# Optimization experiments

Measured on AMD Instinct MI355X. Metric: run time of the kernel, lower is better.

Reference implementation:

```python
import jax, jax.numpy as jnp
import numpy as np

# dims: L=seq_len, N=batch, C=embed_dim, H=heads, D=head_dim, W=window_size
L, N, C, H, D, W = 1024, 4, 2048, 16, 128, 512
ROPE_BASE = 10000.0
SCALE = 1.0 / np.sqrt(D).astype(np.float32)


def _rope(x, cos, sin):
    # interleaved-pair rotary embedding; x: (..., D), cos/sin broadcast to (..., D//2)
    x1, x2 = x[..., 0::2], x[..., 1::2]
    return jnp.stack([x1 * cos - x2 * sin, x1 * sin + x2 * cos], axis=-1).reshape(x.shape)


def setup_inputs() -> dict:
    key = jax.random.key(0)
    ks = jax.random.split(key, 4)
    s = 0.02
    return {
        "x": jax.random.normal(ks[0], (L, N, C), jnp.float32),
        "wq": jax.random.normal(ks[1], (C, C), jnp.float32) * s,
        "bq": jnp.zeros((C,), jnp.float32),
        "wkv": jax.random.normal(ks[2], (2 * C, C), jnp.float32) * s,
        "bkv": jnp.zeros((2 * C,), jnp.float32),
        "wo": jax.random.normal(ks[3], (C, C), jnp.float32) * s,
        "bo": jnp.zeros((C,), jnp.float32),
        "alibi_slopes": jnp.asarray(2.0 ** (-8.0 * np.arange(1, H + 1) / H), jnp.float32),
    }


def reference(x, wq, bq, wkv, bkv, wo, bo, alibi_slopes):
    # x: (L, N, C) -> batch-major (N, L, C)
    xb = jnp.transpose(x, (1, 0, 2))
    q = (xb @ wq.T + bq).reshape(N, L, H, D)
    # memory=None path: zero input cache, cache_mask all False
    cache = jnp.zeros((N, W, C), x.dtype)
    kv_cache = cache @ wkv.T + bkv          # detached in original; masked out anyway
    kv_cur = xb @ wkv.T + bkv
    kv = jnp.concatenate([kv_cache, kv_cur], axis=1).reshape(N, L + W, 2, H, D)
    # RoPE over absolute kv positions [0, L+W); queries live at positions [W, W+L)
    t = jnp.arange(L + W, dtype=jnp.float32)
    inv_freq = 1.0 / (ROPE_BASE ** (jnp.arange(0, D, 2, dtype=jnp.float32) / D))
    freqs = jnp.outer(t, inv_freq)          # (L+W, D//2)
    cos, sin = jnp.cos(freqs), jnp.sin(freqs)
    q = _rope(q, cos[W:W + L][None, :, None, :], sin[W:W + L][None, :, None, :])
    k = _rope(kv[:, :, 0], cos[None, :, None, :], sin[None, :, None, :])
    v = kv[:, :, 1]
    scores = jnp.einsum('bihd,bjhd->bhij', q, k) * SCALE  # (N,H,L,L+W)
    i = jnp.arange(L)[:, None]
    j = jnp.arange(L + W)[None, :]
    # causal sliding window: query at kv-position i+W attends j in [i, i+W];
    # kv_mask is False for the (empty) cache region j < W
    mask = (j >= i) & (j <= i + W) & (j >= W)
    bias = alibi_slopes[:, None, None] * (j - i - W).astype(jnp.float32)  # <= 0 in window
    scores = jnp.where(mask[None, None], scores + bias[None], -jnp.inf)
    p = jax.nn.softmax(scores, axis=-1)
    attn = jnp.einsum('bhij,bjhd->bihd', p, v).reshape(N, L, C)
    out = attn @ wo.T + bo
    return jnp.transpose(out, (1, 0, 2))    # (L, N, C)
```

## Files before the change

### kernel.cpp

```cpp
#include <hip/hip_runtime.h>
#include <hip/hip_bf16.h>

typedef __attribute__((ext_vector_type(4))) float f32x4;
typedef __attribute__((ext_vector_type(8))) short s16x8;
typedef __attribute__((ext_vector_type(4))) short s16x4;
typedef __attribute__((ext_vector_type(4))) int i32x4;

__device__ __forceinline__ short f2bf(float f) {
    union { __hip_bfloat16 h; short s; } u;
    u.h = __float2bfloat16(f);
    return u.s;
}

#define GLD16(g, l) __builtin_amdgcn_global_load_lds((const __attribute__((address_space(1))) void*)(g), (__attribute__((address_space(3))) void*)(l), 16, 0, 0)
#define MFMA16(a, b, c) __builtin_amdgcn_mfma_f32_16x16x32_bf16((a), (b), (c), 0, 0, 0)

__global__ void conv_lin(const float* __restrict__ in, short* __restrict__ out, int n4) {
    int i = blockIdx.x * blockDim.x + threadIdx.x;
    int stride = gridDim.x * blockDim.x;
    for (; i < n4; i += stride) {
        float4 v = reinterpret_cast<const float4*>(in)[i];
        s16x4 o;
        o[0] = f2bf(v.x); o[1] = f2bf(v.y); o[2] = f2bf(v.z); o[3] = f2bf(v.w);
        reinterpret_cast<s16x4*>(out)[i] = o;
    }
}

__global__ void conv_x(const float* __restrict__ x, short* __restrict__ Xb) {
    const int total = 1024 * 4 * 2048 / 4;
    int i = blockIdx.x * blockDim.x + threadIdx.x;
    int stride = gridDim.x * blockDim.x;
    for (; i < total; i += stride) {
        float4 v = reinterpret_cast<const float4*>(x)[i];
        int c4 = i & 511;
        int n  = (i >> 9) & 3;
        int l  = i >> 11;
        s16x4 o;
        o[0] = f2bf(v.x); o[1] = f2bf(v.y); o[2] = f2bf(v.z); o[3] = f2bf(v.w);
        reinterpret_cast<s16x4*>(Xb)[(n * 1024 + l) * 512 + c4] = o;
    }
}

__global__ void rope_tab(float* __restrict__ ctab, float* __restrict__ stab) {
    int l = blockIdx.x, t = threadIdx.x;
    float pos = (float)(512 + l);
    float inv = __expf(-9.210340371976184f * ((float)t * (1.0f / 64.0f)));
    float a = pos * inv;
    float s, c;
    sincosf(a, &s, &c);
    ctab[l * 64 + t] = c;
    stab[l * 64 + t] = s;
}

__device__ __forceinline__ void gemm128(const short* __restrict__ A, const short* __restrict__ B,
                                        short* As, short* Bs, f32x4 acc[4][4], int m0, int j0) {
    const int K = 2048;
    const int tid = threadIdx.x;
    const int lane = tid & 63;
    const int w = tid >> 6;
    const int wr = w >> 1, wc = w & 1;
    const int r8 = lane >> 3;
    const int cc = ((lane & 7) ^ r8) << 3;
    const size_t rowA0 = (size_t)(m0 + w * 32 + r8);
    const size_t rowB0 = (size_t)(j0 + w * 32 + r8);
    for (int kt = 0; kt < K; kt += 64) {
        #pragma unroll
        for (int q = 0; q < 4; ++q) {
            GLD16(A + (rowA0 + q * 8) * K + kt + cc, As + (w * 32 + q * 8) * 64);
            GLD16(B + (rowB0 + q * 8) * K + kt + cc, Bs + (w * 32 + q * 8) * 64);
        }
        __syncthreads();
        #pragma unroll
        for (int kk = 0; kk < 2; ++kk) {
            s16x8 af[4], bfv[4];
            #pragma unroll
            for (int mi = 0; mi < 4; ++mi) {
                int row = wr * 64 + mi * 16 + (lane & 15);
                int byte = row * 128 + ((kk * 64 + (lane >> 4) * 16) ^ ((row & 7) << 4));
                af[mi] = *reinterpret_cast<const s16x8*>(reinterpret_cast<const char*>(As) + byte);
            }
            #pragma unroll
            for (int nj = 0; nj < 4; ++nj) {
                int row = wc * 64 + nj * 16 + (lane & 15);
                int byte = row * 128 + ((kk * 64 + (lane >> 4) * 16) ^ ((row & 7) << 4));
                bfv[nj] = *reinterpret_cast<const s16x8*>(reinterpret_cast<const char*>(Bs) + byte);
            }
            #pragma unroll
            for (int mi = 0; mi < 4; ++mi)
                #pragma unroll
                for (int nj = 0; nj < 4; ++nj)
                    acc[mi][nj] = MFMA16(af[mi], bfv[nj], acc[mi][nj]);
        }
        __syncthreads();
    }
}

__global__ __launch_bounds__(256, 2)
void gemm_qkv(const short* __restrict__ Xb, const short* __restrict__ Wqkv,
              const float* __restrict__ bq, const float* __restrict__ bkv,
              const float* __restrict__ ctab, const float* __restrict__ stab,
              short* __restrict__ Qr, short* __restrict__ Kr, short* __restrict__ Vr) {
    __shared__ short As[8192], Bs[8192];
    const int m0 = blockIdx.y * 128, j0 = blockIdx.x * 128;
    f32x4 acc[4][4];
    #pragma unroll
    for (int a = 0; a < 4; ++a)
        #pragma unroll
        for (int b = 0; b < 4; ++b)
            #pragma unroll
            for (int r = 0; r < 4; ++r) acc[a][b][r] = 0.f;
    gemm128(Xb, Wqkv, As, Bs, acc, m0, j0);

    const int tid = threadIdx.x, lane = tid & 63, w = tid >> 6;
    const int wr = w >> 1, wc = w & 1;
    const int region = j0 >> 11;
    #pragma unroll
    for (int mi = 0; mi < 4; ++mi) {
        #pragma unroll
        for (int nj = 0; nj < 4; ++nj) {
            int col = j0 + wc * 64 + nj * 16 + (lane & 15);
            int h = (col >> 7) & 15;
            int d = col & 127;
            #pragma unroll
            for (int r = 0; r < 4; ++r) {
                int row = m0 + wr * 64 + mi * 16 + (lane >> 4) * 4 + r;
                int n = row >> 10, l = row & 1023;
                float v = acc[mi][nj][r];
                size_t oidx = (((size_t)(n * 16 + h)) * 1024 + l) * 128 + d;
                if (region == 0) {
                    v += bq[col];
                    float other = __shfl_xor(v, 1, 64);
                    float cs = ctab[l * 64 + (d >> 1)];
                    float sn = stab[l * 64 + (d >> 1)];
                    float o = (d & 1) ? (other * sn + v * cs) : (v * cs - other * sn);
                    Qr[oidx] = f2bf(o * 0.08838834764831843f);
                } else if (region == 1) {
                    v += bkv[col - 2048];
                    float other = __shfl_xor(v, 1, 64);
                    float cs = ctab[l * 64 + (d >> 1)];
                    float sn = stab[l * 64 + (d >> 1)];
                    float o = (d & 1) ? (other * sn + v * cs) : (v * cs - other * sn);
                    Kr[oidx] = f2bf(o);
                } else {
                    v += bkv[col - 2048];
                    Vr[oidx] = f2bf(v);
                }
            }
        }
    }
}

__global__ __launch_bounds__(256, 1)
void attn_fwd(const short* __restrict__ Qr, const short* __restrict__ Kr,
              const short* __restrict__ Vr, const float* __restrict__ slopes,
              short* __restrict__ Attn) {
    __shared__ short Ks[64 * 128];
    __shared__ short Vts[128 * 64];
    __shared__ short Ps[4][2048];

    const int i0 = blockIdx.x * 128;
    const int nh = blockIdx.y;
    const int n = nh >> 4, h = nh & 15;
    const short* Qh = Qr + (size_t)nh * (1024 * 128);
    const short* Kh = Kr + (size_t)nh * (1024 * 128);
    const short* Vh = Vr + (size_t)nh * (1024 * 128);
    const float slope = slopes[h];
    const int tid = threadIdx.x, lane = tid & 63, w = tid >> 6;

    s16x8 qf[2][4];
    #pragma unroll
    for (int mi = 0; mi < 2; ++mi)
        #pragma unroll
        for (int kk = 0; kk < 4; ++kk) {
            int row = i0 + w * 32 + mi * 16 + (lane & 15);
            qf[mi][kk] = *reinterpret_cast<const s16x8*>(Qh + (size_t)row * 128 + kk * 32 + (lane >> 4) * 8);
        }

    f32x4 oacc[2][8];
    #pragma unroll
    for (int mi = 0; mi < 2; ++mi)
        #pragma unroll
        for (int dj = 0; dj < 8; ++dj)
            #pragma unroll
            for (int r = 0; r < 4; ++r) oacc[mi][dj][r] = 0.f;
    float mrun[2][4], lrun[2][4];
    #pragma unroll
    for (int mi = 0; mi < 2; ++mi)
        #pragma unroll
        for (int r = 0; r < 4; ++r) { mrun[mi][r] = -1e30f; lrun[mi][r] = 0.f; }

    const int jlo = (i0 >= 512) ? (i0 - 512) : 0;
    const int jhi = i0 + 127;
    for (int j0 = jlo; j0 <= jhi; j0 += 64) {
        #pragma unroll
        for (int q = 0; q < 4; ++q) {
            int rbase = w * 16 + q * 4;
            int rloc = rbase + (lane >> 4);
            int lc = ((lane & 15) ^ (rloc & 7)) << 3;
            GLD16(Kh + (size_t)(j0 + rloc) * 128 + lc, Ks + rbase * 128);
        }
        #pragma unroll
        for (int p = 0; p < 4; ++p) {
            int d0 = (w + p * 4) * 8;
            int jj = j0 + lane;
            i32x4 vv = *reinterpret_cast<const i32x4*>(Vh + (size_t)jj * 128 + d0);
            const short* vs = reinterpret_cast<const short*>(&vv);
            #pragma unroll
            for (int e = 0; e < 8; ++e) {
                int d = d0 + e;
                int byte = d * 128 + ((lane * 2) ^ ((d & 7) << 4));
                *reinterpret_cast<short*>(reinterpret_cast<char*>(Vts) + byte) = vs[e];
            }
        }
        __syncthreads();

        f32x4 sacc[2][4];
        #pragma unroll
        for (int mi = 0; mi < 2; ++mi)
            #pragma unroll
            for (int nj = 0; nj < 4; ++nj)
                #pragma unroll
                for (int r = 0; r < 4; ++r) sacc[mi][nj][r] = 0.f;
        #pragma unroll
        for (int kk = 0; kk < 4; ++kk) {
            s16x8 kf[4];
            #pragma unroll
            for (int nj = 0; nj < 4; ++nj) {
                int kr = nj * 16 + (lane & 15);
                int byte = kr * 256 + ((kk * 64 + (lane >> 4) * 16) ^ ((kr & 7) << 4));
                kf[nj] = *reinterpret_cast<const s16x8*>(reinterpret_cast<const char*>(Ks) + byte);
            }
            #pragma unroll
            for (int mi = 0; mi < 2; ++mi)
                #pragma unroll
                for (int nj = 0; nj < 4; ++nj)
                    sacc[mi][nj] = MFMA16(qf[mi][kk], kf[nj], sacc[mi][nj]);
        }

        #pragma unroll
        for (int mi = 0; mi < 2; ++mi) {
            #pragma unroll
            for (int r = 0; r < 4; ++r) {
                int iq = i0 + w * 32 + mi * 16 + (lane >> 4) * 4 + r;
                float mx = -1e30f;
                #pragma unroll
                for (int nj = 0; nj < 4; ++nj) {
                    int jj = j0 + nj * 16 + (lane & 15);
                    float v = -1e30f;
                    if (jj <= iq && jj >= iq - 512)
                        v = sacc[mi][nj][r] + slope * (float)(jj - iq);
                    sacc[mi][nj][r] = v;
                    mx = fmaxf(mx, v);
                }
                #pragma unroll
                for (int s = 1; s < 16; s <<= 1) mx = fmaxf(mx, __shfl_xor(mx, s, 64));
                float mnew = fmaxf(mrun[mi][r], mx);
                float sf = __expf(mrun[mi][r] - mnew);
                mrun[mi][r] = mnew;
                lrun[mi][r] *= sf;
                #pragma unroll
                for (int dj = 0; dj < 8; ++dj) oacc[mi][dj][r] *= sf;
                float rs = 0.f;
                #pragma unroll
                for (int nj = 0; nj < 4; ++nj) {
                    float v = sacc[mi][nj][r];
                    float p = (v < -1e29f) ? 0.f : __expf(v - mnew);
                    sacc[mi][nj][r] = p;
                    rs += p;
                }
                #pragma unroll
                for (int s = 1; s < 16; s <<= 1) rs += __shfl_xor(rs, s, 64);
                lrun[mi][r] += rs;
            }
        }

        char* Pw = reinterpret_cast<char*>(&Ps[w][0]);
        #pragma unroll
        for (int mi = 0; mi < 2; ++mi)
            #pragma unroll
            for (int nj = 0; nj < 4; ++nj)
                #pragma unroll
                for (int r = 0; r < 4; ++r) {
                    int prow = mi * 16 + (lane >> 4) * 4 + r;
                    int cb = (nj * 16 + (lane & 15)) * 2;
                    int byte = prow * 128 + (cb ^ ((prow & 7) << 4));
                    *reinterpret_cast<short*>(Pw + byte) = f2bf(sacc[mi][nj][r]);
                }

        #pragma unroll
        for (int ks = 0; ks < 2; ++ks) {
            s16x8 pf[2];
            #pragma unroll
            for (int mi = 0; mi < 2; ++mi) {
                int prow = mi * 16 + (lane & 15);
                int byte = prow * 128 + (((ks * 32 + (lane >> 4) * 8) * 2) ^ ((prow & 7) << 4));
                pf[mi] = *reinterpret_cast<const s16x8*>(Pw + byte);
            }
            #pragma unroll
            for (int dj = 0; dj < 8; ++dj) {
                int d = dj * 16 + (lane & 15);
                int byte = d * 128 + (((ks * 32 + (lane >> 4) * 8) * 2) ^ ((d & 7) << 4));
                s16x8 vf = *reinterpret_cast<const s16x8*>(reinterpret_cast<const char*>(Vts) + byte);
                #pragma unroll
                for (int mi = 0; mi < 2; ++mi)
                    oacc[mi][dj] = MFMA16(pf[mi], vf, oacc[mi][dj]);
            }
        }
        __syncthreads();
    }

    #pragma unroll
    for (int mi = 0; mi < 2; ++mi)
        #pragma unroll
        for (int dj = 0; dj < 8; ++dj)
            #pragma unroll
            for (int r = 0; r < 4; ++r) {
                int iq = i0 + w * 32 + mi * 16 + (lane >> 4) * 4 + r;
                int d = dj * 16 + (lane & 15);
                float v = oacc[mi][dj][r] / lrun[mi][r];
                Attn[((size_t)(n * 1024 + iq)) * 2048 + h * 128 + d] = f2bf(v);
            }
}

__global__ __launch_bounds__(256, 2)
void gemm_out(const short* __restrict__ Attn, const short* __restrict__ Wo,
              const float* __restrict__ bo, float* __restrict__ out) {
    __shared__ short As[8192], Bs[8192];
    const int m0 = blockIdx.y * 128, j0 = blockIdx.x * 128;
    f32x4 acc[4][4];
    #pragma unroll
    for (int a = 0; a < 4; ++a)
        #pragma unroll
        for (int b = 0; b < 4; ++b)
            #pragma unroll
            for (int r = 0; r < 4; ++r) acc[a][b][r] = 0.f;
    gemm128(Attn, Wo, As, Bs, acc, m0, j0);

    const int tid = threadIdx.x, lane = tid & 63, w = tid >> 6;
    const int wr = w >> 1, wc = w & 1;
    #pragma unroll
    for (int mi = 0; mi < 4; ++mi)
        #pragma unroll
        for (int nj = 0; nj < 4; ++nj) {
            int col = j0 + wc * 64 + nj * 16 + (lane & 15);
            #pragma unroll
            for (int r = 0; r < 4; ++r) {
                int row = m0 + wr * 64 + mi * 16 + (lane >> 4) * 4 + r;
                int n = row >> 10, l = row & 1023;
                out[((size_t)(l * 4 + n)) * 2048 + col] = acc[mi][nj][r] + bo[col];
            }
        }
}

extern "C" void kernel_launch(void* const* d_in, const int* in_sizes, int n_in,
                              void* d_out, int out_size, void* d_ws, size_t ws_size,
                              hipStream_t stream) {
    const float* x      = (const float*)d_in[0];
    const float* wq     = (const float*)d_in[1];
    const float* bq     = (const float*)d_in[2];
    const float* wkv    = (const float*)d_in[3];
    const float* bkv    = (const float*)d_in[4];
    const float* wo     = (const float*)d_in[5];
    const float* bo     = (const float*)d_in[6];
    const float* slopes = (const float*)d_in[7];
    float* out = (float*)d_out;

    char* ws = (char*)d_ws;
    size_t off = 0;
    auto alloc = [&](size_t bytes) { char* p = ws + off; off += (bytes + 255) & ~(size_t)255; return p; };
    float* ctab = (float*)alloc((size_t)1024 * 64 * 4);
    float* stab = (float*)alloc((size_t)1024 * 64 * 4);
    short* Xb   = (short*)alloc((size_t)4096 * 2048 * 2);
    short* Wqkv = (short*)alloc((size_t)6144 * 2048 * 2);
    short* Wo   = (short*)alloc((size_t)2048 * 2048 * 2);
    short* Qr   = (short*)alloc((size_t)64 * 1024 * 128 * 2);
    short* Kr   = (short*)alloc((size_t)64 * 1024 * 128 * 2);
    short* Vr   = (short*)alloc((size_t)64 * 1024 * 128 * 2);
    short* Attn = (short*)alloc((size_t)4096 * 2048 * 2);

    conv_x<<<2048, 256, 0, stream>>>(x, Xb);
    conv_lin<<<1024, 256, 0, stream>>>(wq, Wqkv, 2048 * 2048 / 4);
    conv_lin<<<2048, 256, 0, stream>>>(wkv, Wqkv + (size_t)2048 * 2048, 4096 * 2048 / 4);
    conv_lin<<<1024, 256, 0, stream>>>(wo, Wo, 2048 * 2048 / 4);
    rope_tab<<<1024, 64, 0, stream>>>(ctab, stab);
    gemm_qkv<<<dim3(48, 32), 256, 0, stream>>>(Xb, Wqkv, bq, bkv, ctab, stab, Qr, Kr, Vr);
    attn_fwd<<<dim3(8, 64), 256, 0, stream>>>(Qr, Kr, Vr, slopes, Attn);
    gemm_out<<<dim3(16, 32), 256, 0, stream>>>(Attn, Wo, bo, out);
}
```

Baseline: 269.7 us.

## Rewrite QKV GEMM as 256x256 tile, 8-wave, 4-stage LDS pipeline

Replaces the 128x128 QKV projection GEMM with a 256x256-tile kernel using 512 threads, a 4-slot ring of 32-wide K slices in LDS, and prefetch of future slices interleaved with MFMA phases. It adds s_setprio around the MFMA blocks and remaps block indices so consecutive blocks share row tiles for L2 reuse. The goal is to hide global-to-LDS latency and double arithmetic intensity per tile. In exchange it uses more registers (32 accumulator tiles per wave) and more LDS, and launches only 384 blocks, which may leave compute units underfilled or reduce occupancy.

After: 345.3 us. 1.28x slower.

```diff
diff --git a/kernel.cpp b/kernel.cpp
--- a/kernel.cpp
+++ b/kernel.cpp
@@ -52,70 +52,100 @@
     stab[l * 64 + t] = s;
 }
 
-__device__ __forceinline__ void gemm128(const short* __restrict__ A, const short* __restrict__ B,
-                                        short* As, short* Bs, f32x4 acc[4][4], int m0, int j0) {
-    const int K = 2048;
-    const int tid = threadIdx.x;
-    const int lane = tid & 63;
-    const int w = tid >> 6;
-    const int wr = w >> 1, wc = w & 1;
-    const int r8 = lane >> 3;
-    const int cc = ((lane & 7) ^ r8) << 3;
-    const size_t rowA0 = (size_t)(m0 + w * 32 + r8);
-    const size_t rowB0 = (size_t)(j0 + w * 32 + r8);
-    for (int kt = 0; kt < K; kt += 64) {
-        #pragma unroll
-        for (int q = 0; q < 4; ++q) {
-            GLD16(A + (rowA0 + q * 8) * K + kt + cc, As + (w * 32 + q * 8) * 64);
-            GLD16(B + (rowB0 + q * 8) * K + kt + cc, Bs + (w * 32 + q * 8) * 64);
-        }
-        __syncthreads();
-        #pragma unroll
-        for (int kk = 0; kk < 2; ++kk) {
-            s16x8 af[4], bfv[4];
-            #pragma unroll
-            for (int mi = 0; mi < 4; ++mi) {
-                int row = wr * 64 + mi * 16 + (lane & 15);
-                int byte = row * 128 + ((kk * 64 + (lane >> 4) * 16) ^ ((row & 7) << 4));
-                af[mi] = *reinterpret_cast<const s16x8*>(reinterpret_cast<const char*>(As) + byte);
-            }
-            #pragma unroll
-            for (int nj = 0; nj < 4; ++nj) {
-                int row = wc * 64 + nj * 16 + (lane & 15);
-                int byte = row * 128 + ((kk * 64 + (lane >> 4) * 16) ^ ((row & 7) << 4));
-                bfv[nj] = *reinterpret_cast<const s16x8*>(reinterpret_cast<const char*>(Bs) + byte);
-            }
-            #pragma unroll
-            for (int mi = 0; mi < 4; ++mi)
-                #pragma unroll
-                for (int nj = 0; nj < 4; ++nj)
-                    acc[mi][nj] = MFMA16(af[mi], bfv[nj], acc[mi][nj]);
-        }
-        __syncthreads();
-    }
-}
-
-__global__ __launch_bounds__(256, 2)
-void gemm_qkv(const short* __restrict__ Xb, const short* __restrict__ Wqkv,
-              const float* __restrict__ bq, const float* __restrict__ bkv,
-              const float* __restrict__ ctab, const float* __restrict__ stab,
-              short* __restrict__ Qr, short* __restrict__ Kr, short* __restrict__ Vr) {
-    __shared__ short As[8192], Bs[8192];
-    const int m0 = blockIdx.y * 128, j0 = blockIdx.x * 128;
-    f32x4 acc[4][4];
-    #pragma unroll
-    for (int a = 0; a < 4; ++a)
-        #pragma unroll
-        for (int b = 0; b < 4; ++b)
-            #pragma unroll
-            for (int r = 0; r < 4; ++r) acc[a][b][r] = 0.f;
-    gemm128(Xb, Wqkv, As, Bs, acc, m0, j0);
-
+__device__ __forceinline__ void stage_half(const short* __restrict__ Gbase, int rowbase, int g,
+                                           short* slot, int tid) {
+    #pragma unroll
+    for (int q = 0; q < 2; ++q) {
+        int chunk = q * 512 + tid;
+        int row = chunk >> 2;
+        int cb = (chunk & 3) * 16;
+        int scb = cb ^ (((row >> 2) & 3) << 4);
+        const short* src = Gbase + (size_t)(rowbase + row) * 2048 + g * 32 + (scb >> 1);
+        GLD16(src, slot + (q * 512 + (tid & ~63)) * 8);
+    }
+}
+
+__device__ __forceinline__ s16x8 read_frag(const short* slot, int row, int lane) {
+    int cb = (lane >> 4) * 16;
+    int byte = row * 64 + (cb ^ (((row >> 2) & 3) << 4));
+    return *reinterpret_cast<const s16x8*>(reinterpret_cast<const char*>(slot) + byte);
+}
+
+#define BAR2() do { __builtin_amdgcn_s_barrier(); __builtin_amdgcn_sched_barrier(0); } while (0)
+
+#define PHASE(Asl, Bsl, MQ, LOADB, STBASE, STROW, STG, STSLOT, ACQ)                         \
+    {                                                                                        \
+        _Pragma("unroll")                                                                    \
+        for (int mi2 = 0; mi2 < 4; ++mi2)                                                    \
+            af[mi2] = read_frag(Asl, wr * 128 + MQ * 64 + mi2 * 16 + (lane & 15), lane);     \
+        if (LOADB) {                                                                         \
+            _Pragma("unroll")                                                                \
+            for (int nj = 0; nj < 4; ++nj)                                                   \
+                bf[nj] = read_frag(Bsl, wc * 64 + nj * 16 + (lane & 15), lane);              \
+        }                                                                                    \
+        stage_half(STBASE, STROW, STG, STSLOT, tid);                                         \
+        __builtin_amdgcn_s_barrier();                                                        \
+        __builtin_amdgcn_sched_barrier(0);                                                   \
+        __builtin_amdgcn_s_setprio(1);                                                       \
+        _Pragma("unroll")                                                                    \
+        for (int mi2 = 0; mi2 < 4; ++mi2)                                                    \
+            _Pragma("unroll")                                                                \
+            for (int nj = 0; nj < 4; ++nj)                                                   \
+                acc[ACQ + mi2][nj] = MFMA16(af[mi2], bf[nj], acc[ACQ + mi2][nj]);            \
+        __builtin_amdgcn_s_setprio(0);                                                       \
+    }
+
+__global__ __launch_bounds__(512, 2)
+void gemm_qkv8(const short* __restrict__ Xb, const short* __restrict__ Wqkv,
+               const float* __restrict__ bq, const float* __restrict__ bkv,
+               const float* __restrict__ ctab, const float* __restrict__ stab,
+               short* __restrict__ Qr, short* __restrict__ Kr, short* __restrict__ Vr) {
+    __shared__ short Al[4][256 * 32];
+    __shared__ short Bl[4][256 * 32];
     const int tid = threadIdx.x, lane = tid & 63, w = tid >> 6;
-    const int wr = w >> 1, wc = w & 1;
+    const int wr = w >> 2, wc = w & 3;
+
+    int b = blockIdx.x;
+    int work = (b & 7) * 48 + (b >> 3);
+    const int m0 = (work & 15) * 256;
+    const int j0 = (work >> 4) * 256;
+
+    f32x4 acc[8][4];
+    #pragma unroll
+    for (int a = 0; a < 8; ++a)
+        #pragma unroll
+        for (int c = 0; c < 4; ++c)
+            #pragma unroll
+            for (int r = 0; r < 4; ++r) acc[a][c][r] = 0.f;
+
+    stage_half(Xb,   m0, 0, Al[0], tid);
+    stage_half(Wqkv, j0, 0, Bl[0], tid);
+    stage_half(Xb,   m0, 1, Al[1], tid);
+    stage_half(Wqkv, j0, 1, Bl[1], tid);
+    stage_half(Xb,   m0, 2, Al[2], tid);
+    stage_half(Wqkv, j0, 2, Bl[2], tid);
+    asm volatile("s_waitcnt vmcnt(4)" ::: "memory");
+    BAR2();
+
+    for (int t = 0; t < 32; ++t) {
+        const int g0 = 2 * t, g1 = 2 * t + 1;
+        const short* As0 = Al[g0 & 3]; const short* Bs0 = Bl[g0 & 3];
+        const short* As1 = Al[g1 & 3]; const short* Bs1 = Bl[g1 & 3];
+        const int ga = (2 * t + 3) & 63;
+        const int gb = (2 * t + 4) & 63;
+        s16x8 af[4], bf[4];
+        PHASE(As0, Bs0, 0, true,  Xb,   m0, ga, Al[ga & 3], 0); BAR2();
+        PHASE(As0, Bs0, 1, false, Wqkv, j0, ga, Bl[ga & 3], 4); BAR2();
+        PHASE(As1, Bs1, 0, true,  Xb,   m0, gb, Al[gb & 3], 0); BAR2();
+        PHASE(As1, Bs1, 1, false, Wqkv, j0, gb, Bl[gb & 3], 4);
+        asm volatile("s_waitcnt vmcnt(4)" ::: "memory");
+        BAR2();
+    }
+    asm volatile("s_waitcnt vmcnt(0)" ::: "memory");
+
     const int region = j0 >> 11;
     #pragma unroll
-    for (int mi = 0; mi < 4; ++mi) {
+    for (int mi = 0; mi < 8; ++mi) {
         #pragma unroll
         for (int nj = 0; nj < 4; ++nj) {
             int col = j0 + wc * 64 + nj * 16 + (lane & 15);
@@ -123,7 +153,7 @@
             int d = col & 127;
             #pragma unroll
             for (int r = 0; r < 4; ++r) {
-                int row = m0 + wr * 64 + mi * 16 + (lane >> 4) * 4 + r;
+                int row = m0 + wr * 128 + mi * 16 + (lane >> 4) * 4 + r;
                 int n = row >> 10, l = row & 1023;
                 float v = acc[mi][nj][r];
                 size_t oidx = (((size_t)(n * 16 + h)) * 1024 + l) * 128 + d;
@@ -150,6 +180,49 @@
     }
 }
 
+__device__ __forceinline__ void gemm128(const short* __restrict__ A, const short* __restrict__ B,
+                                        short* As, short* Bs, f32x4 acc[4][4], int m0, int j0) {
+    const int K = 2048;
+    const int tid = threadIdx.x;
+    const int lane = tid & 63;
+    const int w = tid >> 6;
+    const int wr = w >> 1, wc = w & 1;
+    const int r8 = lane >> 3;
+    const int cc = ((lane & 7) ^ r8) << 3;
+    const size_t rowA0 = (size_t)(m0 + w * 32 + r8);
+    const size_t rowB0 = (size_t)(j0 + w * 32 + r8);
+    for (int kt = 0; kt < K; kt += 64) {
+        #pragma unroll
+        for (int q = 0; q < 4; ++q) {
+            GLD16(A + (rowA0 + q * 8) * K + kt + cc, As + (w * 32 + q * 8) * 64);
+            GLD16(B + (rowB0 + q * 8) * K + kt + cc, Bs + (w * 32 + q * 8) * 64);
+        }
+        __syncthreads();
+        #pragma unroll
+        for (int kk = 0; kk < 2; ++kk) {
+            s16x8 af[4], bfv[4];
+            #pragma unroll
+            for (int mi = 0; mi < 4; ++mi) {
+                int row = wr * 64 + mi * 16 + (lane & 15);
+                int byte = row * 128 + ((kk * 64 + (lane >> 4) * 16) ^ ((row & 7) << 4));
+                af[mi] = *reinterpret_cast<const s16x8*>(reinterpret_cast<const char*>(As) + byte);
+            }
+            #pragma unroll
+            for (int nj = 0; nj < 4; ++nj) {
+                int row = wc * 64 + nj * 16 + (lane & 15);
+                int byte = row * 128 + ((kk * 64 + (lane >> 4) * 16) ^ ((row & 7) << 4));
+                bfv[nj] = *reinterpret_cast<const s16x8*>(reinterpret_cast<const char*>(Bs) + byte);
+            }
+            #pragma unroll
+            for (int mi = 0; mi < 4; ++mi)
+                #pragma unroll
+                for (int nj = 0; nj < 4; ++nj)
+                    acc[mi][nj] = MFMA16(af[mi], bfv[nj], acc[mi][nj]);
+        }
+        __syncthreads();
+    }
+}
+
 __global__ __launch_bounds__(256, 1)
 void attn_fwd(const short* __restrict__ Qr, const short* __restrict__ Kr,
               const short* __restrict__ Vr, const float* __restrict__ slopes,
@@ -383,7 +456,7 @@
     conv_lin<<<2048, 256, 0, stream>>>(wkv, Wqkv + (size_t)2048 * 2048, 4096 * 2048 / 4);
     conv_lin<<<1024, 256, 0, stream>>>(wo, Wo, 2048 * 2048 / 4);
     rope_tab<<<1024, 64, 0, stream>>>(ctab, stab);
-    gemm_qkv<<<dim3(48, 32), 256, 0, stream>>>(Xb, Wqkv, bq, bkv, ctab, stab, Qr, Kr, Vr);
+    gemm_qkv8<<<384, 512, 0, stream>>>(Xb, Wqkv, bq, bkv, ctab, stab, Qr, Kr, Vr);
     attn_fwd<<<dim3(8, 64), 256, 0, stream>>>(Qr, Kr, Vr, slopes, Attn);
     gemm_out<<<dim3(16, 32), 256, 0, stream>>>(Attn, Wo, bo, out);
 }
```

## Double-buffer GEMM LDS tiles with 256x128 blocks and remapped block order

Applied to the files above, without the earlier changes.

Replaces the single-buffered 128x128 GEMM mainloop with a double-buffered 256x128 tile core on 512 threads. The next K-slice is prefetched via global_load_lds while MFMAs run on the current one, and s_setprio raises wave priority around the MFMA bursts. Block indices are remapped so consecutive blocks spread across the grid, aiming at better L2 reuse. The cost is more LDS per block (96KB), which limits occupancy, and both QKV and output projection GEMMs are affected.

New measurement: 288.6 us. 7.0% more time.

```diff
diff --git a/kernel.cpp b/kernel.cpp
--- a/kernel.cpp
+++ b/kernel.cpp
@@ -52,64 +52,90 @@
     stab[l * 64 + t] = s;
 }
 
-__device__ __forceinline__ void gemm128(const short* __restrict__ A, const short* __restrict__ B,
-                                        short* As, short* Bs, f32x4 acc[4][4], int m0, int j0) {
-    const int K = 2048;
-    const int tid = threadIdx.x;
-    const int lane = tid & 63;
-    const int w = tid >> 6;
-    const int wr = w >> 1, wc = w & 1;
-    const int r8 = lane >> 3;
-    const int cc = ((lane & 7) ^ r8) << 3;
-    const size_t rowA0 = (size_t)(m0 + w * 32 + r8);
-    const size_t rowB0 = (size_t)(j0 + w * 32 + r8);
-    for (int kt = 0; kt < K; kt += 64) {
-        #pragma unroll
-        for (int q = 0; q < 4; ++q) {
-            GLD16(A + (rowA0 + q * 8) * K + kt + cc, As + (w * 32 + q * 8) * 64);
-            GLD16(B + (rowB0 + q * 8) * K + kt + cc, Bs + (w * 32 + q * 8) * 64);
-        }
-        __syncthreads();
-        #pragma unroll
-        for (int kk = 0; kk < 2; ++kk) {
-            s16x8 af[4], bfv[4];
-            #pragma unroll
-            for (int mi = 0; mi < 4; ++mi) {
-                int row = wr * 64 + mi * 16 + (lane & 15);
-                int byte = row * 128 + ((kk * 64 + (lane >> 4) * 16) ^ ((row & 7) << 4));
-                af[mi] = *reinterpret_cast<const s16x8*>(reinterpret_cast<const char*>(As) + byte);
-            }
-            #pragma unroll
-            for (int nj = 0; nj < 4; ++nj) {
-                int row = wc * 64 + nj * 16 + (lane & 15);
-                int byte = row * 128 + ((kk * 64 + (lane >> 4) * 16) ^ ((row & 7) << 4));
-                bfv[nj] = *reinterpret_cast<const s16x8*>(reinterpret_cast<const char*>(Bs) + byte);
-            }
-            #pragma unroll
-            for (int mi = 0; mi < 4; ++mi)
-                #pragma unroll
-                for (int nj = 0; nj < 4; ++nj)
-                    acc[mi][nj] = MFMA16(af[mi], bfv[nj], acc[mi][nj]);
-        }
+
+__device__ __forceinline__ void stage_t(const short* __restrict__ G, int rowbase, int kt,
+                                        short* dst, int tid, int q) {
+    int chunk = q * 512 + tid;
+    int row = chunk >> 3;
+    int c = ((chunk & 7) << 4) ^ ((row & 7) << 4);
+    GLD16(G + (size_t)(rowbase + row) * 2048 + kt + (c >> 1), dst + (q * 512 + (tid & ~63)) * 8);
+}
+
+__device__ __forceinline__ s16x8 rd_frag(const short* buf, int row, int ks, int lane) {
+    int byte = row * 128 + (((ks << 6) + ((lane >> 4) << 4)) ^ ((row & 7) << 4));
+    return *reinterpret_cast<const s16x8*>(reinterpret_cast<const char*>(buf) + byte);
+}
+
+__device__ __forceinline__ void gemm_core(const short* __restrict__ A, const short* __restrict__ B,
+                                          short* Ab0, short* Ab1, short* Bb0, short* Bb1,
+                                          f32x4 acc[4][4], int m0, int j0) {
+    const int tid = threadIdx.x, lane = tid & 63;
+    const int w = tid >> 6, wr = w >> 1, wc = w & 1;
+
+    stage_t(A, m0, 0, Ab0, tid, 0); stage_t(A, m0, 0, Ab0, tid, 1);
+    stage_t(A, m0, 0, Ab0, tid, 2); stage_t(A, m0, 0, Ab0, tid, 3);
+    stage_t(B, j0, 0, Bb0, tid, 0); stage_t(B, j0, 0, Bb0, tid, 1);
+    __syncthreads();
+
+    for (int t = 0; t < 32; ++t) {
+        const short* As = (t & 1) ? Ab1 : Ab0;
+        const short* Bs = (t & 1) ? Bb1 : Bb0;
+        short* An = (t & 1) ? Ab0 : Ab1;
+        short* Bn = (t & 1) ? Bb0 : Bb1;
+        const int ktn = (t + 1) << 6;
+        const bool pf = (t < 31);
+
+        s16x8 a0[4], b0[4];
+        #pragma unroll
+        for (int mi = 0; mi < 4; ++mi) a0[mi] = rd_frag(As, wr * 64 + mi * 16 + (lane & 15), 0, lane);
+        #pragma unroll
+        for (int nj = 0; nj < 4; ++nj) b0[nj] = rd_frag(Bs, wc * 64 + nj * 16 + (lane & 15), 0, lane);
+        if (pf) { stage_t(A, m0, ktn, An, tid, 0); stage_t(A, m0, ktn, An, tid, 1); }
+        __builtin_amdgcn_s_setprio(1);
+        #pragma unroll
+        for (int mi = 0; mi < 4; ++mi)
+            #pragma unroll
+            for (int nj = 0; nj < 4; ++nj)
+                acc[mi][nj] = MFMA16(a0[mi], b0[nj], acc[mi][nj]);
+        __builtin_amdgcn_s_setprio(0);
+        if (pf) { stage_t(A, m0, ktn, An, tid, 2); stage_t(A, m0, ktn, An, tid, 3); }
+
+        s16x8 a1[4], b1[4];
+        #pragma unroll
+        for (int mi = 0; mi < 4; ++mi) a1[mi] = rd_frag(As, wr * 64 + mi * 16 + (lane & 15), 1, lane);
+        #pragma unroll
+        for (int nj = 0; nj < 4; ++nj) b1[nj] = rd_frag(Bs, wc * 64 + nj * 16 + (lane & 15), 1, lane);
+        if (pf) { stage_t(B, j0, ktn, Bn, tid, 0); stage_t(B, j0, ktn, Bn, tid, 1); }
+        __builtin_amdgcn_s_setprio(1);
+        #pragma unroll
+        for (int mi = 0; mi < 4; ++mi)
+            #pragma unroll
+            for (int nj = 0; nj < 4; ++nj)
+                acc[mi][nj] = MFMA16(a1[mi], b1[nj], acc[mi][nj]);
+        __builtin_amdgcn_s_setprio(0);
         __syncthreads();
     }
 }
 
-__global__ __launch_bounds__(256, 2)
-void gemm_qkv(const short* __restrict__ Xb, const short* __restrict__ Wqkv,
-              const float* __restrict__ bq, const float* __restrict__ bkv,
-              const float* __restrict__ ctab, const float* __restrict__ stab,
-              short* __restrict__ Qr, short* __restrict__ Kr, short* __restrict__ Vr) {
-    __shared__ short As[8192], Bs[8192];
-    const int m0 = blockIdx.y * 128, j0 = blockIdx.x * 128;
+__global__ __launch_bounds__(512, 2)
+void gemm_qkv2(const short* __restrict__ Xb, const short* __restrict__ Wqkv,
+               const float* __restrict__ bq, const float* __restrict__ bkv,
+               const float* __restrict__ ctab, const float* __restrict__ stab,
+               short* __restrict__ Qr, short* __restrict__ Kr, short* __restrict__ Vr) {
+    __shared__ short Ab0[256 * 64], Ab1[256 * 64], Bb0[128 * 64], Bb1[128 * 64];
+    int b = blockIdx.x;
+    int work = (b & 7) * 96 + (b >> 3);
+    const int m0 = (work & 15) * 256;
+    const int j0 = (work >> 4) * 128;
+
     f32x4 acc[4][4];
     #pragma unroll
     for (int a = 0; a < 4; ++a)
         #pragma unroll
-        for (int b = 0; b < 4; ++b)
-            #pragma unroll
-            for (int r = 0; r < 4; ++r) acc[a][b][r] = 0.f;
-    gemm128(Xb, Wqkv, As, Bs, acc, m0, j0);
+        for (int c = 0; c < 4; ++c)
+            #pragma unroll
+            for (int r = 0; r < 4; ++r) acc[a][c][r] = 0.f;
+    gemm_core(Xb, Wqkv, Ab0, Ab1, Bb0, Bb1, acc, m0, j0);
 
     const int tid = threadIdx.x, lane = tid & 63, w = tid >> 6;
     const int wr = w >> 1, wc = w & 1;
@@ -150,6 +176,40 @@
     }
 }
 
+__global__ __launch_bounds__(512, 2)
+void gemm_out2(const short* __restrict__ Attn, const short* __restrict__ Wo,
+               const float* __restrict__ bo, float* __restrict__ out) {
+    __shared__ short Ab0[256 * 64], Ab1[256 * 64], Bb0[128 * 64], Bb1[128 * 64];
+    int b = blockIdx.x;
+    int work = (b & 7) * 32 + (b >> 3);
+    const int m0 = (work & 15) * 256;
+    const int j0 = (work >> 4) * 128;
+
+    f32x4 acc[4][4];
+    #pragma unroll
+    for (int a = 0; a < 4; ++a)
+        #pragma unroll
+        for (int c = 0; c < 4; ++c)
+            #pragma unroll
+            for (int r = 0; r < 4; ++r) acc[a][c][r] = 0.f;
+    gemm_core(Attn, Wo, Ab0, Ab1, Bb0, Bb1, acc, m0, j0);
+
+    const int tid = threadIdx.x, lane = tid & 63, w = tid >> 6;
+    const int wr = w >> 1, wc = w & 1;
+    #pragma unroll
+    for (int mi = 0; mi < 4; ++mi)
+        #pragma unroll
+        for (int nj = 0; nj < 4; ++nj) {
+            int col = j0 + wc * 64 + nj * 16 + (lane & 15);
+            #pragma unroll
+            for (int r = 0; r < 4; ++r) {
+                int row = m0 + wr * 64 + mi * 16 + (lane >> 4) * 4 + r;
+                int n = row >> 10, l = row & 1023;
+                out[((size_t)(l * 4 + n)) * 2048 + col] = acc[mi][nj][r] + bo[col];
+            }
+        }
+}
+
 __global__ __launch_bounds__(256, 1)
 void attn_fwd(const short* __restrict__ Qr, const short* __restrict__ Kr,
               const short* __restrict__ Vr, const float* __restrict__ slopes,
@@ -320,36 +380,6 @@
                 float v = oacc[mi][dj][r] / lrun[mi][r];
                 Attn[((size_t)(n * 1024 + iq)) * 2048 + h * 128 + d] = f2bf(v);
             }
-}
-
-__global__ __launch_bounds__(256, 2)
-void gemm_out(const short* __restrict__ Attn, const short* __restrict__ Wo,
-              const float* __restrict__ bo, float* __restrict__ out) {
-    __shared__ short As[8192], Bs[8192];
-    const int m0 = blockIdx.y * 128, j0 = blockIdx.x * 128;
-    f32x4 acc[4][4];
-    #pragma unroll
-    for (int a = 0; a < 4; ++a)
-        #pragma unroll
-        for (int b = 0; b < 4; ++b)
-            #pragma unroll
-            for (int r = 0; r < 4; ++r) acc[a][b][r] = 0.f;
-    gemm128(Attn, Wo, As, Bs, acc, m0, j0);
-
-    const int tid = threadIdx.x, lane = tid & 63, w = tid >> 6;
-    const int wr = w >> 1, wc = w & 1;
-    #pragma unroll
-    for (int mi = 0; mi < 4; ++mi)
-        #pragma unroll
-        for (int nj = 0; nj < 4; ++nj) {
-            int col = j0 + wc * 64 + nj * 16 + (lane & 15);
-            #pragma unroll
-            for (int r = 0; r < 4; ++r) {
-                int row = m0 + wr * 64 + mi * 16 + (lane >> 4) * 4 + r;
-                int n = row >> 10, l = row & 1023;
-                out[((size_t)(l * 4 + n)) * 2048 + col] = acc[mi][nj][r] + bo[col];
-            }
-        }
 }
 
 extern "C" void kernel_launch(void* const* d_in, const int* in_sizes, int n_in,
@@ -383,7 +413,7 @@
     conv_lin<<<2048, 256, 0, stream>>>(wkv, Wqkv + (size_t)2048 * 2048, 4096 * 2048 / 4);
     conv_lin<<<1024, 256, 0, stream>>>(wo, Wo, 2048 * 2048 / 4);
     rope_tab<<<1024, 64, 0, stream>>>(ctab, stab);
-    gemm_qkv<<<dim3(48, 32), 256, 0, stream>>>(Xb, Wqkv, bq, bkv, ctab, stab, Qr, Kr, Vr);
+    gemm_qkv2<<<768, 512, 0, stream>>>(Xb, Wqkv, bq, bkv, ctab, stab, Qr, Kr, Vr);
     attn_fwd<<<dim3(8, 64), 256, 0, stream>>>(Qr, Kr, Vr, slopes, Attn);
-    gemm_out<<<dim3(16, 32), 256, 0, stream>>>(Attn, Wo, bo, out);
-}
+    gemm_out2<<<256, 512, 0, stream>>>(Attn, Wo, bo, out);
+}
```

## Double-buffer GEMM LDS tiles with async prefetch and remap attention grid

Applied to the files above, without the earlier changes.

The shared GEMM mainloop now double-buffers the A/B tiles in LDS. It issues global-to-LDS loads for the next K tile before computing the current one, uses explicit vmcnt waits and raw barriers, and raises wave priority around the MFMA block. This is meant to hide global load latency behind matrix math, at the cost of doubling LDS per block (64KB), which may limit the two-blocks-per-CU occupancy. Separately, the attention launch becomes a 1D grid that interleaves heads and batches, so concurrently running blocks are spread across different (n,h) pairs, which may change L2 and XCD locality.

Measured after the change: 285.2 us. +5.7%, slower.

```diff
diff --git a/kernel.cpp b/kernel.cpp
--- a/kernel.cpp
+++ b/kernel.cpp
@@ -52,8 +52,8 @@
     stab[l * 64 + t] = s;
 }
 
-__device__ __forceinline__ void gemm128(const short* __restrict__ A, const short* __restrict__ B,
-                                        short* As, short* Bs, f32x4 acc[4][4], int m0, int j0) {
+__device__ __forceinline__ void gemm128p(const short* __restrict__ A, const short* __restrict__ B,
+                                         short* As, short* Bs, f32x4 acc[4][4], int m0, int j0) {
     const int K = 2048;
     const int tid = threadIdx.x;
     const int lane = tid & 63;
@@ -63,13 +63,31 @@
     const int cc = ((lane & 7) ^ r8) << 3;
     const size_t rowA0 = (size_t)(m0 + w * 32 + r8);
     const size_t rowB0 = (size_t)(j0 + w * 32 + r8);
-    for (int kt = 0; kt < K; kt += 64) {
-        #pragma unroll
-        for (int q = 0; q < 4; ++q) {
-            GLD16(A + (rowA0 + q * 8) * K + kt + cc, As + (w * 32 + q * 8) * 64);
-            GLD16(B + (rowB0 + q * 8) * K + kt + cc, Bs + (w * 32 + q * 8) * 64);
-        }
-        __syncthreads();
+
+    #pragma unroll
+    for (int q = 0; q < 4; ++q) {
+        GLD16(A + (rowA0 + q * 8) * K + cc, As + (w * 32 + q * 8) * 64);
+        GLD16(B + (rowB0 + q * 8) * K + cc, Bs + (w * 32 + q * 8) * 64);
+    }
+
+    for (int t = 0; t < 32; ++t) {
+        const short* Asr = As + (t & 1) * 8192;
+        const short* Bsr = Bs + (t & 1) * 8192;
+        if (t < 31) {
+            short* Asn = As + ((t + 1) & 1) * 8192;
+            short* Bsn = Bs + ((t + 1) & 1) * 8192;
+            const int kt = (t + 1) << 6;
+            #pragma unroll
+            for (int q = 0; q < 4; ++q) {
+                GLD16(A + (rowA0 + q * 8) * K + kt + cc, Asn + (w * 32 + q * 8) * 64);
+                GLD16(B + (rowB0 + q * 8) * K + kt + cc, Bsn + (w * 32 + q * 8) * 64);
+            }
+            asm volatile("s_waitcnt vmcnt(8)" ::: "memory");
+        } else {
+            asm volatile("s_waitcnt vmcnt(0)" ::: "memory");
+        }
+        __builtin_amdgcn_s_barrier();
+        __builtin_amdgcn_sched_barrier(0);
         #pragma unroll
         for (int kk = 0; kk < 2; ++kk) {
             s16x8 af[4], bfv[4];
@@ -77,21 +95,24 @@
             for (int mi = 0; mi < 4; ++mi) {
                 int row = wr * 64 + mi * 16 + (lane & 15);
                 int byte = row * 128 + ((kk * 64 + (lane >> 4) * 16) ^ ((row & 7) << 4));
-                af[mi] = *reinterpret_cast<const s16x8*>(reinterpret_cast<const char*>(As) + byte);
+                af[mi] = *reinterpret_cast<const s16x8*>(reinterpret_cast<const char*>(Asr) + byte);
             }
             #pragma unroll
             for (int nj = 0; nj < 4; ++nj) {
                 int row = wc * 64 + nj * 16 + (lane & 15);
                 int byte = row * 128 + ((kk * 64 + (lane >> 4) * 16) ^ ((row & 7) << 4));
-                bfv[nj] = *reinterpret_cast<const s16x8*>(reinterpret_cast<const char*>(Bs) + byte);
-            }
+                bfv[nj] = *reinterpret_cast<const s16x8*>(reinterpret_cast<const char*>(Bsr) + byte);
+            }
+            __builtin_amdgcn_s_setprio(1);
             #pragma unroll
             for (int mi = 0; mi < 4; ++mi)
                 #pragma unroll
                 for (int nj = 0; nj < 4; ++nj)
                     acc[mi][nj] = MFMA16(af[mi], bfv[nj], acc[mi][nj]);
-        }
-        __syncthreads();
+            __builtin_amdgcn_s_setprio(0);
+        }
+        __builtin_amdgcn_s_barrier();
+        __builtin_amdgcn_sched_barrier(0);
     }
 }
 
@@ -100,7 +121,7 @@
               const float* __restrict__ bq, const float* __restrict__ bkv,
               const float* __restrict__ ctab, const float* __restrict__ stab,
               short* __restrict__ Qr, short* __restrict__ Kr, short* __restrict__ Vr) {
-    __shared__ short As[8192], Bs[8192];
+    __shared__ short As[16384], Bs[16384];
     const int m0 = blockIdx.y * 128, j0 = blockIdx.x * 128;
     f32x4 acc[4][4];
     #pragma unroll
@@ -109,7 +130,7 @@
         for (int b = 0; b < 4; ++b)
             #pragma unroll
             for (int r = 0; r < 4; ++r) acc[a][b][r] = 0.f;
-    gemm128(Xb, Wqkv, As, Bs, acc, m0, j0);
+    gemm128p(Xb, Wqkv, As, Bs, acc, m0, j0);
 
     const int tid = threadIdx.x, lane = tid & 63, w = tid >> 6;
     const int wr = w >> 1, wc = w & 1;
@@ -150,6 +171,36 @@
     }
 }
 
+__global__ __launch_bounds__(256, 2)
+void gemm_out(const short* __restrict__ Attn, const short* __restrict__ Wo,
+              const float* __restrict__ bo, float* __restrict__ out) {
+    __shared__ short As[16384], Bs[16384];
+    const int m0 = blockIdx.y * 128, j0 = blockIdx.x * 128;
+    f32x4 acc[4][4];
+    #pragma unroll
+    for (int a = 0; a < 4; ++a)
+        #pragma unroll
+        for (int b = 0; b < 4; ++b)
+            #pragma unroll
+            for (int r = 0; r < 4; ++r) acc[a][b][r] = 0.f;
+    gemm128p(Attn, Wo, As, Bs, acc, m0, j0);
+
+    const int tid = threadIdx.x, lane = tid & 63, w = tid >> 6;
+    const int wr = w >> 1, wc = w & 1;
+    #pragma unroll
+    for (int mi = 0; mi < 4; ++mi)
+        #pragma unroll
+        for (int nj = 0; nj < 4; ++nj) {
+            int col = j0 + wc * 64 + nj * 16 + (lane & 15);
+            #pragma unroll
+            for (int r = 0; r < 4; ++r) {
+                int row = m0 + wr * 64 + mi * 16 + (lane >> 4) * 4 + r;
+                int n = row >> 10, l = row & 1023;
+                out[((size_t)(l * 4 + n)) * 2048 + col] = acc[mi][nj][r] + bo[col];
+            }
+        }
+}
+
 __global__ __launch_bounds__(256, 1)
 void attn_fwd(const short* __restrict__ Qr, const short* __restrict__ Kr,
               const short* __restrict__ Vr, const float* __restrict__ slopes,
@@ -158,8 +209,9 @@
     __shared__ short Vts[128 * 64];
     __shared__ short Ps[4][2048];
 
-    const int i0 = blockIdx.x * 128;
-    const int nh = blockIdx.y;
+    const int b = blockIdx.x;
+    const int nh = (b & 7) * 8 + ((b >> 3) & 7);
+    const int i0 = (b >> 6) * 128;
     const int n = nh >> 4, h = nh & 15;
     const short* Qh = Qr + (size_t)nh * (1024 * 128);
     const short* Kh = Kr + (size_t)nh * (1024 * 128);
@@ -320,36 +372,6 @@
                 float v = oacc[mi][dj][r] / lrun[mi][r];
                 Attn[((size_t)(n * 1024 + iq)) * 2048 + h * 128 + d] = f2bf(v);
             }
-}
-
-__global__ __launch_bounds__(256, 2)
-void gemm_out(const short* __restrict__ Attn, const short* __restrict__ Wo,
-              const float* __restrict__ bo, float* __restrict__ out) {
-    __shared__ short As[8192], Bs[8192];
-    const int m0 = blockIdx.y * 128, j0 = blockIdx.x * 128;
-    f32x4 acc[4][4];
-    #pragma unroll
-    for (int a = 0; a < 4; ++a)
-        #pragma unroll
-        for (int b = 0; b < 4; ++b)
-            #pragma unroll
-            for (int r = 0; r < 4; ++r) acc[a][b][r] = 0.f;
-    gemm128(Attn, Wo, As, Bs, acc, m0, j0);
-
-    const int tid = threadIdx.x, lane = tid & 63, w = tid >> 6;
-    const int wr = w >> 1, wc = w & 1;
-    #pragma unroll
-    for (int mi = 0; mi < 4; ++mi)
-        #pragma unroll
-        for (int nj = 0; nj < 4; ++nj) {
-            int col = j0 + wc * 64 + nj * 16 + (lane & 15);
-            #pragma unroll
-            for (int r = 0; r < 4; ++r) {
-                int row = m0 + wr * 64 + mi * 16 + (lane >> 4) * 4 + r;
-                int n = row >> 10, l = row & 1023;
-                out[((size_t)(l * 4 + n)) * 2048 + col] = acc[mi][nj][r] + bo[col];
-            }
-        }
 }
 
 extern "C" void kernel_launch(void* const* d_in, const int* in_sizes, int n_in,
@@ -384,6 +406,6 @@
     conv_lin<<<1024, 256, 0, stream>>>(wo, Wo, 2048 * 2048 / 4);
     rope_tab<<<1024, 64, 0, stream>>>(ctab, stab);
     gemm_qkv<<<dim3(48, 32), 256, 0, stream>>>(Xb, Wqkv, bq, bkv, ctab, stab, Qr, Kr, Vr);
-    attn_fwd<<<dim3(8, 64), 256, 0, stream>>>(Qr, Kr, Vr, slopes, Attn);
+    attn_fwd<<<512, 256, 0, stream>>>(Qr, Kr, Vr, slopes, Attn);
     gemm_out<<<dim3(16, 32), 256, 0, stream>>>(Attn, Wo, bo, out);
 }
```
